# Optimization experiments

Measured on AMD Instinct MI355X. Metric: run time of the kernel, lower is better.

The kernel has to match this reference:

```python
import jax, jax.numpy as jnp
import numpy as np

D_MODEL = 1024
NUM_HEADS = 16
D_K = D_MODEL // NUM_HEADS


def setup_inputs() -> dict:
    key = jax.random.key(0)
    ks = jax.random.split(key, 11)
    s = 1.0 / np.sqrt(D_MODEL)
    inp = {
        "Q": jax.random.normal(ks[0], (2, 2048, D_MODEL), jnp.float32),
        "K": jax.random.normal(ks[1], (2, 2048, D_MODEL), jnp.float32),
        "V": jax.random.normal(ks[2], (2, 2048, D_MODEL), jnp.float32),
        "W_q": jax.random.uniform(ks[3], (D_MODEL, D_MODEL), jnp.float32, -s, s),
        "b_q": jax.random.uniform(ks[4], (D_MODEL,), jnp.float32, -s, s),
        "W_k": jax.random.uniform(ks[5], (D_MODEL, D_MODEL), jnp.float32, -s, s),
        "b_k": jax.random.uniform(ks[6], (D_MODEL,), jnp.float32, -s, s),
        "W_v": jax.random.uniform(ks[7], (D_MODEL, D_MODEL), jnp.float32, -s, s),
        "b_v": jax.random.uniform(ks[8], (D_MODEL,), jnp.float32, -s, s),
        "W_o": jax.random.uniform(ks[9], (D_MODEL, D_MODEL), jnp.float32, -s, s),
        "b_o": jax.random.uniform(ks[10], (D_MODEL,), jnp.float32, -s, s),
    }
    return inp


def reference(Q, K, V, W_q, b_q, W_k, b_k, W_v, b_v, W_o, b_o):
    B, S, _ = Q.shape
    # Linear projections (torch Linear: x @ W.T + b; W here stored as [in, out])
    q = Q @ W_q + b_q
    k = K @ W_k + b_k
    v = V @ W_v + b_v
    # split heads -> [B, H, S, d_k]
    q = q.reshape(B, S, NUM_HEADS, D_K).transpose(0, 2, 1, 3)
    k = k.reshape(B, S, NUM_HEADS, D_K).transpose(0, 2, 1, 3)
    v = v.reshape(B, S, NUM_HEADS, D_K).transpose(0, 2, 1, 3)
    scale = 1.0 / np.sqrt(D_K).astype(np.float32)
    scores = jnp.einsum('bhqd,bhkd->bhqk', q, k) * scale  # [B,H,S,S]
    probs = jax.nn.softmax(scores, axis=-1)
    attn = jnp.einsum('bhqk,bhkd->bhqd', probs, v)  # [B,H,S,d_k]
    attn = attn.transpose(0, 2, 1, 3).reshape(B, S, D_MODEL)
    return attn @ W_o + b_o
```

## Files before the change

kernel.cpp:

```cpp
#include <hip/hip_runtime.h>
#include <math.h>

#define SEQ   2048
#define DM    1024
#define NH    16
#define DK    64
#define MTOT  4096
#define QSCALE 0.18033688011112043f

typedef __bf16 bf16x8 __attribute__((ext_vector_type(8)));
typedef float  f32x4  __attribute__((ext_vector_type(4)));
typedef unsigned short u16;

__device__ __forceinline__ u16 f2bf(float f) {
    unsigned int u = __float_as_uint(f);
    u += 0x7fff + ((u >> 16) & 1);
    return (u16)(u >> 16);
}

__device__ __forceinline__ void async16(const void* g, void* l) {
    __builtin_amdgcn_global_load_lds(
        (const __attribute__((address_space(1))) unsigned int*)(unsigned long long)g,
        (__attribute__((address_space(3))) unsigned int*)(unsigned int)(unsigned long long)l,
        16, 0, 0);
}

__device__ __forceinline__ bf16x8 ld16(const u16* p) {
    bf16x8 v;
    __builtin_memcpy(&v, p, 16);
    return v;
}
__device__ __forceinline__ bf16x8 ld8x2(const u16* p) {
    union { unsigned long long q[2]; bf16x8 v; } u;
    __builtin_memcpy(&u.q[0], p, 8);
    __builtin_memcpy(&u.q[1], p + 4, 8);
    return u.v;
}
__device__ __forceinline__ void st8(u16* p, unsigned int lo, unsigned int hi) {
    unsigned long long q = ((unsigned long long)hi << 32) | lo;
    __builtin_memcpy(p, &q, 8);
}

__global__ __launch_bounds__(256)
void cvt_in(const float* __restrict__ Q, const float* __restrict__ K,
            const float* __restrict__ V, u16* __restrict__ Qb,
            u16* __restrict__ Kb, u16* __restrict__ Vb)
{
    const float* src; u16* dst;
    if (blockIdx.z == 0)      { src = Q; dst = Qb; }
    else if (blockIdx.z == 1) { src = K; dst = Kb; }
    else                      { src = V; dst = Vb; }
    const size_t i = ((size_t)blockIdx.x * 256 + threadIdx.x) * 8;
    float4 a = *(const float4*)&src[i];
    float4 b = *(const float4*)&src[i + 4];
    uint4 o;
    o.x = (unsigned)f2bf(a.x) | ((unsigned)f2bf(a.y) << 16);
    o.y = (unsigned)f2bf(a.z) | ((unsigned)f2bf(a.w) << 16);
    o.z = (unsigned)f2bf(b.x) | ((unsigned)f2bf(b.y) << 16);
    o.w = (unsigned)f2bf(b.z) | ((unsigned)f2bf(b.w) << 16);
    *(uint4*)&dst[i] = o;
}

__global__ __launch_bounds__(256)
void cvt_wt(const float* __restrict__ Wq, const float* __restrict__ Wk,
            const float* __restrict__ Wv, const float* __restrict__ Wo,
            u16* __restrict__ Tq, u16* __restrict__ Tk,
            u16* __restrict__ Tv, u16* __restrict__ To)
{
    const float* W; u16* Wt;
    if (blockIdx.z == 0)      { W = Wq; Wt = Tq; }
    else if (blockIdx.z == 1) { W = Wk; Wt = Tk; }
    else if (blockIdx.z == 2) { W = Wv; Wt = Tv; }
    else                      { W = Wo; Wt = To; }
    __shared__ float Ts[64][65];
    const int t = threadIdx.x;
    const int k0 = blockIdx.x * 64, n0 = blockIdx.y * 64;
#pragma unroll
    for (int p = 0; p < 4; ++p) {
        const int flat = t + p * 256;
        const int r = flat >> 4, c4 = (flat & 15) * 4;
        float4 v = *(const float4*)&W[(size_t)(k0 + r) * DM + n0 + c4];
        Ts[r][c4 + 0] = v.x; Ts[r][c4 + 1] = v.y;
        Ts[r][c4 + 2] = v.z; Ts[r][c4 + 3] = v.w;
    }
    __syncthreads();
#pragma unroll
    for (int p = 0; p < 2; ++p) {
        const int flat = t + p * 256;
        const int n = flat >> 3, kc = (flat & 7) * 8;
        uint4 o;
        o.x = (unsigned)f2bf(Ts[kc + 0][n]) | ((unsigned)f2bf(Ts[kc + 1][n]) << 16);
        o.y = (unsigned)f2bf(Ts[kc + 2][n]) | ((unsigned)f2bf(Ts[kc + 3][n]) << 16);
        o.z = (unsigned)f2bf(Ts[kc + 4][n]) | ((unsigned)f2bf(Ts[kc + 5][n]) << 16);
        o.w = (unsigned)f2bf(Ts[kc + 6][n]) | ((unsigned)f2bf(Ts[kc + 7][n]) << 16);
        *(uint4*)&Wt[(size_t)(n0 + n) * DM + k0 + kc] = o;
    }
}

__global__ __launch_bounds__(256)
void v_transpose(const u16* __restrict__ vn, u16* __restrict__ vt)
{
    __shared__ u16 Ts[64][65];
    const int t = threadIdx.x;
    const int s0 = blockIdx.x * 64, bh = blockIdx.y;
    const size_t nb = (size_t)bh * SEQ * DK;
#pragma unroll
    for (int p = 0; p < 2; ++p) {
        const int flat = t + p * 256;
        const int r = flat >> 3, c = (flat & 7) * 8;
        union { uint4 u; u16 s[8]; } v;
        v.u = *(const uint4*)&vn[nb + (size_t)(s0 + r) * DK + c];
#pragma unroll
        for (int j = 0; j < 8; ++j) Ts[r][c + j] = v.s[j];
    }
    __syncthreads();
#pragma unroll
    for (int p = 0; p < 2; ++p) {
        const int flat = t + p * 256;
        const int d = flat >> 3, sc = (flat & 7) * 8;
        union { uint4 u; u16 s[8]; } v;
#pragma unroll
        for (int j = 0; j < 8; ++j) v.s[j] = Ts[sc + j][d];
        *(uint4*)&vt[nb + (size_t)d * SEQ + s0 + sc] = v.u;
    }
}

template <int SCATTER>
__device__ __forceinline__ void gemm_core(const u16* __restrict__ A,
                                          const u16* __restrict__ Wt,
                                          const float* __restrict__ bias,
                                          void* __restrict__ Out, float scale)
{
    __shared__ u16 As[128 * 32];
    __shared__ u16 Bs[128 * 32];

    const int tid = threadIdx.x;
    const int lane = tid & 63;
    const int wv = __builtin_amdgcn_readfirstlane(tid >> 6);
    const int wm = wv >> 1, wn = wv & 1;
    const int lane15 = lane & 15, quad = lane >> 4;
    const int row0 = blockIdx.x * 128, col0 = blockIdx.y * 128;

    const int arow = lane >> 2;
    const int acol = (lane & 3) * 8;

    f32x4 acc[4][4];
#pragma unroll
    for (int i = 0; i < 4; ++i)
#pragma unroll
        for (int j = 0; j < 4; ++j) acc[i][j] = (f32x4)0.f;

    for (int k0 = 0; k0 < DM; k0 += 32) {
#pragma unroll
        for (int cc = 0; cc < 2; ++cc) {
            const int c = 2 * wv + cc;
            async16(&A[(size_t)(row0 + c * 16 + arow) * DM + k0 + acol],
                    &As[c * 512]);
            async16(&Wt[(size_t)(col0 + c * 16 + arow) * DM + k0 + acol],
                    &Bs[c * 512]);
        }
        __syncthreads();

        bf16x8 af[4];
#pragma unroll
        for (int mi = 0; mi < 4; ++mi)
            af[mi] = ld16(&As[(wm * 64 + mi * 16 + lane15) * 32 + quad * 8]);
#pragma unroll
        for (int ni = 0; ni < 4; ++ni) {
            bf16x8 bfrag = ld16(&Bs[(wn * 64 + ni * 16 + lane15) * 32 + quad * 8]);
#pragma unroll
            for (int mi = 0; mi < 4; ++mi)
                acc[mi][ni] = __builtin_amdgcn_mfma_f32_16x16x32_bf16(
                    af[mi], bfrag, acc[mi][ni], 0, 0, 0);
        }
        __syncthreads();
    }

#pragma unroll
    for (int mi = 0; mi < 4; ++mi) {
        const int mbase = row0 + wm * 64 + mi * 16 + quad * 4;
#pragma unroll
        for (int ni = 0; ni < 4; ++ni) {
            const int n = col0 + wn * 64 + ni * 16 + lane15;
            const float bz = bias[n];
            if (SCATTER) {
                const int h = n >> 6, dk = n & 63;
#pragma unroll
                for (int r = 0; r < 4; ++r) {
                    const int mm = mbase + r;
                    const int b_ = mm >> 11, s = mm & 2047;
                    ((u16*)Out)[(((size_t)(b_ * NH + h)) * SEQ + s) * DK + dk] =
                        f2bf((acc[mi][ni][r] + bz) * scale);
                }
            } else {
#pragma unroll
                for (int r = 0; r < 4; ++r) {
                    const int mm = mbase + r;
                    ((float*)Out)[(size_t)mm * DM + n] = acc[mi][ni][r] + bz;
                }
            }
        }
    }
}

__global__ __launch_bounds__(256)
void qkv_gemm(const u16* __restrict__ Qb, const u16* __restrict__ Kb,
              const u16* __restrict__ Vb,
              const u16* __restrict__ Tq, const u16* __restrict__ Tk,
              const u16* __restrict__ Tv,
              const float* __restrict__ bq, const float* __restrict__ bk,
              const float* __restrict__ bv,
              u16* __restrict__ qw, u16* __restrict__ kw, u16* __restrict__ vw)
{
    if (blockIdx.z == 0)      gemm_core<1>(Qb, Tq, bq, qw, QSCALE);
    else if (blockIdx.z == 1) gemm_core<1>(Kb, Tk, bk, kw, 1.0f);
    else                      gemm_core<1>(Vb, Tv, bv, vw, 1.0f);
}

__global__ __launch_bounds__(256)
void out_gemm(const u16* __restrict__ A, const u16* __restrict__ To,
              const float* __restrict__ bo, float* __restrict__ Out)
{
    gemm_core<0>(A, To, bo, Out, 1.0f);
}

__global__ __launch_bounds__(256, 4)
void attn_mfma(const u16* __restrict__ qw, const u16* __restrict__ kw,
               const u16* __restrict__ vt, u16* __restrict__ attnb)
{
    __shared__ u16 Qs[64 * 68];
    __shared__ u16 Ks[64 * 68];
    __shared__ u16 Vts[64 * 68];
    __shared__ u16 Ps[4][16 * 68];

    const int tid = threadIdx.x;
    const int lane = tid & 63;
    const int wv = tid >> 6;
    const int lane15 = lane & 15, quad = lane >> 4;
    const int bh = blockIdx.x;
    const int q0 = blockIdx.y * 64;
    const size_t base = (size_t)bh * SEQ * DK;

#pragma unroll
    for (int i = 0; i < 2; ++i) {
        const int flat = tid + i * 256;
        const int r = flat >> 3, c = (flat & 7) * 8;
        uint4 v = *(const uint4*)&qw[base + (size_t)(q0 + r) * DK + c];
        st8(&Qs[r * 68 + c], v.x, v.y);
        st8(&Qs[r * 68 + c + 4], v.z, v.w);
    }
    __syncthreads();

    bf16x8 qa[2];
#pragma unroll
    for (int kk = 0; kk < 2; ++kk)
        qa[kk] = ld8x2(&Qs[(wv * 16 + lane15) * 68 + kk * 32 + quad * 8]);

    u16* Pw = &Ps[wv][0];

    f32x4 o_acc[4];
    float lpart[4];
#pragma unroll
    for (int nd = 0; nd < 4; ++nd) o_acc[nd] = (f32x4)0.f;
#pragma unroll
    for (int r = 0; r < 4; ++r) lpart[r] = 0.f;

    for (int c0 = 0; c0 < SEQ; c0 += 64) {
#pragma unroll
        for (int i = 0; i < 2; ++i) {
            const int flat = tid + i * 256;
            const int r = flat >> 3, c = (flat & 7) * 8;
            uint4 kv = *(const uint4*)&kw[base + (size_t)(c0 + r) * DK + c];
            st8(&Ks[r * 68 + c], kv.x, kv.y);
            st8(&Ks[r * 68 + c + 4], kv.z, kv.w);
            uint4 vv = *(const uint4*)&vt[base + (size_t)r * SEQ + c0 + c];
            st8(&Vts[r * 68 + c], vv.x, vv.y);
            st8(&Vts[r * 68 + c + 4], vv.z, vv.w);
        }
        __syncthreads();

        f32x4 s_acc[4];
#pragma unroll
        for (int ni = 0; ni < 4; ++ni) s_acc[ni] = (f32x4)0.f;
#pragma unroll
        for (int ni = 0; ni < 4; ++ni)
#pragma unroll
            for (int kk = 0; kk < 2; ++kk) {
                bf16x8 kb = ld8x2(&Ks[(ni * 16 + lane15) * 68 + kk * 32 + quad * 8]);
                s_acc[ni] = __builtin_amdgcn_mfma_f32_16x16x32_bf16(
                    qa[kk], kb, s_acc[ni], 0, 0, 0);
            }

#pragma unroll
        for (int ni = 0; ni < 4; ++ni) {
#pragma unroll
            for (int r = 0; r < 4; ++r) {
                const float p = exp2f(s_acc[ni][r]);
                lpart[r] += p;
                Pw[(quad * 4 + r) * 68 + ni * 16 + lane15] = f2bf(p);
            }
        }

        bf16x8 pa[2];
#pragma unroll
        for (int kk = 0; kk < 2; ++kk)
            pa[kk] = ld8x2(&Pw[lane15 * 68 + kk * 32 + quad * 8]);
#pragma unroll
        for (int nd = 0; nd < 4; ++nd)
#pragma unroll
            for (int kk = 0; kk < 2; ++kk) {
                bf16x8 vb = ld8x2(&Vts[(nd * 16 + lane15) * 68 + kk * 32 + quad * 8]);
                o_acc[nd] = __builtin_amdgcn_mfma_f32_16x16x32_bf16(
                    pa[kk], vb, o_acc[nd], 0, 0, 0);
            }
        __syncthreads();
    }

#pragma unroll
    for (int r = 0; r < 4; ++r) {
        float l = lpart[r];
        l += __shfl_xor(l, 1);
        l += __shfl_xor(l, 2);
        l += __shfl_xor(l, 4);
        l += __shfl_xor(l, 8);
        lpart[r] = 1.f / l;
    }

    const int b_ = bh >> 4, h = bh & 15;
#pragma unroll
    for (int r = 0; r < 4; ++r) {
        const int srow = q0 + wv * 16 + quad * 4 + r;
#pragma unroll
        for (int nd = 0; nd < 4; ++nd)
            attnb[((size_t)b_ * SEQ + srow) * DM + h * DK + nd * 16 + lane15] =
                f2bf(o_acc[nd][r] * lpart[r]);
    }
}

extern "C" void kernel_launch(void* const* d_in, const int* in_sizes, int n_in,
                              void* d_out, int out_size, void* d_ws, size_t ws_size,
                              hipStream_t stream)
{
    const float* Q  = (const float*)d_in[0];
    const float* K  = (const float*)d_in[1];
    const float* V  = (const float*)d_in[2];
    const float* Wq = (const float*)d_in[3];
    const float* bq = (const float*)d_in[4];
    const float* Wk = (const float*)d_in[5];
    const float* bk = (const float*)d_in[6];
    const float* Wv = (const float*)d_in[7];
    const float* bv = (const float*)d_in[8];
    const float* Wo = (const float*)d_in[9];
    const float* bo = (const float*)d_in[10];
    float* out = (float*)d_out;

    const size_t MB = 1024 * 1024;
    char* w8 = (char*)d_ws;
    u16* Qbf = (u16*)(w8 + 0 * MB);
    u16* Kbf = (u16*)(w8 + 8 * MB);
    u16* Vbf = (u16*)(w8 + 16 * MB);
    u16* Wtq = (u16*)(w8 + 24 * MB);
    u16* Wtk = (u16*)(w8 + 26 * MB);
    u16* Wtv = (u16*)(w8 + 28 * MB);
    u16* Wto = (u16*)(w8 + 30 * MB);
    u16* qw  = (u16*)(w8 + 32 * MB);
    u16* kw  = (u16*)(w8 + 40 * MB);
    u16* vw  = (u16*)(w8 + 48 * MB);
    u16* vtw = (u16*)(w8 + 56 * MB);
    u16* attnb = Qbf;

    cvt_in<<<dim3(2048, 1, 3), 256, 0, stream>>>(Q, K, V, Qbf, Kbf, Vbf);
    cvt_wt<<<dim3(16, 16, 4), 256, 0, stream>>>(Wq, Wk, Wv, Wo,
                                                Wtq, Wtk, Wtv, Wto);
    qkv_gemm<<<dim3(32, 8, 3), 256, 0, stream>>>(Qbf, Kbf, Vbf, Wtq, Wtk, Wtv,
                                                 bq, bk, bv, qw, kw, vw);
    v_transpose<<<dim3(32, 32), 256, 0, stream>>>(vw, vtw);
    attn_mfma<<<dim3(32, 32), 256, 0, stream>>>(qw, kw, vtw, attnb);
    out_gemm<<<dim3(32, 8), 256, 0, stream>>>(attnb, Wto, bo, out);
}
```

Before: 253.0 us.

## Fuse V transpose into QKV epilogue, enlarge attention Q tile, prefetch K/V

The V projection epilogue now writes its output directly in transposed [B,H,dk,S] layout with packed 8-byte stores, which removes the separate v_transpose kernel and its round trip through memory. The attention kernel now handles 128 query rows per block (two 16-row MFMA tiles per wave), so each K/V tile loaded into shared memory is reused twice as much. It also prefetches the next K/V tile into registers while computing on the current one. The output GEMM uses 128x64 tiles to launch twice as many blocks. The trade-off is higher register pressure in attention, since the occupancy hint was dropped, and fewer attention blocks overall.

```diff
diff --git a/kernel.cpp b/kernel.cpp
--- a/kernel.cpp
+++ b/kernel.cpp
@@ -11,6 +11,7 @@
 typedef __bf16 bf16x8 __attribute__((ext_vector_type(8)));
 typedef float  f32x4  __attribute__((ext_vector_type(4)));
 typedef unsigned short u16;
+typedef unsigned long long u64;
 
 __device__ __forceinline__ u16 f2bf(float f) {
     unsigned int u = __float_as_uint(f);
@@ -31,13 +32,13 @@
     return v;
 }
 __device__ __forceinline__ bf16x8 ld8x2(const u16* p) {
-    union { unsigned long long q[2]; bf16x8 v; } u;
+    union { u64 q[2]; bf16x8 v; } u;
     __builtin_memcpy(&u.q[0], p, 8);
     __builtin_memcpy(&u.q[1], p + 4, 8);
     return u.v;
 }
 __device__ __forceinline__ void st8(u16* p, unsigned int lo, unsigned int hi) {
-    unsigned long long q = ((unsigned long long)hi << 32) | lo;
+    u64 q = ((u64)hi << 32) | lo;
     __builtin_memcpy(p, &q, 8);
 }
 
@@ -97,34 +98,6 @@
     }
 }
 
-__global__ __launch_bounds__(256)
-void v_transpose(const u16* __restrict__ vn, u16* __restrict__ vt)
-{
-    __shared__ u16 Ts[64][65];
-    const int t = threadIdx.x;
-    const int s0 = blockIdx.x * 64, bh = blockIdx.y;
-    const size_t nb = (size_t)bh * SEQ * DK;
-#pragma unroll
-    for (int p = 0; p < 2; ++p) {
-        const int flat = t + p * 256;
-        const int r = flat >> 3, c = (flat & 7) * 8;
-        union { uint4 u; u16 s[8]; } v;
-        v.u = *(const uint4*)&vn[nb + (size_t)(s0 + r) * DK + c];
-#pragma unroll
-        for (int j = 0; j < 8; ++j) Ts[r][c + j] = v.s[j];
-    }
-    __syncthreads();
-#pragma unroll
-    for (int p = 0; p < 2; ++p) {
-        const int flat = t + p * 256;
-        const int d = flat >> 3, sc = (flat & 7) * 8;
-        union { uint4 u; u16 s[8]; } v;
-#pragma unroll
-        for (int j = 0; j < 8; ++j) v.s[j] = Ts[sc + j][d];
-        *(uint4*)&vt[nb + (size_t)d * SEQ + s0 + sc] = v.u;
-    }
-}
-
 template <int SCATTER>
 __device__ __forceinline__ void gemm_core(const u16* __restrict__ A,
                                           const u16* __restrict__ Wt,
@@ -183,7 +156,7 @@
         for (int ni = 0; ni < 4; ++ni) {
             const int n = col0 + wn * 64 + ni * 16 + lane15;
             const float bz = bias[n];
-            if (SCATTER) {
+            if (SCATTER == 1) {
                 const int h = n >> 6, dk = n & 63;
 #pragma unroll
                 for (int r = 0; r < 4; ++r) {
@@ -192,6 +165,16 @@
                     ((u16*)Out)[(((size_t)(b_ * NH + h)) * SEQ + s) * DK + dk] =
                         f2bf((acc[mi][ni][r] + bz) * scale);
                 }
+            } else if (SCATTER == 2) {
+                const int h = n >> 6, dk = n & 63;
+                const int b_ = mbase >> 11, s0 = mbase & 2047;
+                u64 q = (u64)f2bf((acc[mi][ni][0] + bz) * scale)
+                      | ((u64)f2bf((acc[mi][ni][1] + bz) * scale) << 16)
+                      | ((u64)f2bf((acc[mi][ni][2] + bz) * scale) << 32)
+                      | ((u64)f2bf((acc[mi][ni][3] + bz) * scale) << 48);
+                u16* dst = (u16*)Out +
+                    (((size_t)(b_ * NH + h)) * DK + dk) * SEQ + s0;
+                __builtin_memcpy(dst, &q, 8);
             } else {
 #pragma unroll
                 for (int r = 0; r < 4; ++r) {
@@ -210,39 +193,98 @@
               const u16* __restrict__ Tv,
               const float* __restrict__ bq, const float* __restrict__ bk,
               const float* __restrict__ bv,
-              u16* __restrict__ qw, u16* __restrict__ kw, u16* __restrict__ vw)
+              u16* __restrict__ qw, u16* __restrict__ kw, u16* __restrict__ vtw)
 {
     if (blockIdx.z == 0)      gemm_core<1>(Qb, Tq, bq, qw, QSCALE);
     else if (blockIdx.z == 1) gemm_core<1>(Kb, Tk, bk, kw, 1.0f);
-    else                      gemm_core<1>(Vb, Tv, bv, vw, 1.0f);
+    else                      gemm_core<2>(Vb, Tv, bv, vtw, 1.0f);
 }
 
 __global__ __launch_bounds__(256)
-void out_gemm(const u16* __restrict__ A, const u16* __restrict__ To,
-              const float* __restrict__ bo, float* __restrict__ Out)
-{
-    gemm_core<0>(A, To, bo, Out, 1.0f);
-}
-
-__global__ __launch_bounds__(256, 4)
+void out_gemm(const u16* __restrict__ A, const u16* __restrict__ Wt,
+              const float* __restrict__ bias, float* __restrict__ Out)
+{
+    __shared__ u16 As[128 * 32];
+    __shared__ u16 Bs[64 * 32];
+
+    const int tid = threadIdx.x;
+    const int lane = tid & 63;
+    const int wv = __builtin_amdgcn_readfirstlane(tid >> 6);
+    const int wm = wv >> 1, wn = wv & 1;
+    const int lane15 = lane & 15, quad = lane >> 4;
+    const int row0 = blockIdx.x * 128, col0 = blockIdx.y * 64;
+
+    const int arow = lane >> 2;
+    const int acol = (lane & 3) * 8;
+
+    f32x4 acc[4][2];
+#pragma unroll
+    for (int i = 0; i < 4; ++i)
+#pragma unroll
+        for (int j = 0; j < 2; ++j) acc[i][j] = (f32x4)0.f;
+
+    for (int k0 = 0; k0 < DM; k0 += 32) {
+#pragma unroll
+        for (int cc = 0; cc < 2; ++cc) {
+            const int c = 2 * wv + cc;
+            async16(&A[(size_t)(row0 + c * 16 + arow) * DM + k0 + acol],
+                    &As[c * 512]);
+        }
+        async16(&Wt[(size_t)(col0 + wv * 16 + arow) * DM + k0 + acol],
+                &Bs[wv * 512]);
+        __syncthreads();
+
+        bf16x8 af[4];
+#pragma unroll
+        for (int mi = 0; mi < 4; ++mi)
+            af[mi] = ld16(&As[(wm * 64 + mi * 16 + lane15) * 32 + quad * 8]);
+#pragma unroll
+        for (int ni = 0; ni < 2; ++ni) {
+            bf16x8 bfrag = ld16(&Bs[(wn * 32 + ni * 16 + lane15) * 32 + quad * 8]);
+#pragma unroll
+            for (int mi = 0; mi < 4; ++mi)
+                acc[mi][ni] = __builtin_amdgcn_mfma_f32_16x16x32_bf16(
+                    af[mi], bfrag, acc[mi][ni], 0, 0, 0);
+        }
+        __syncthreads();
+    }
+
+#pragma unroll
+    for (int mi = 0; mi < 4; ++mi) {
+        const int mbase = row0 + wm * 64 + mi * 16 + quad * 4;
+#pragma unroll
+        for (int ni = 0; ni < 2; ++ni) {
+            const int n = col0 + wn * 32 + ni * 16 + lane15;
+            const float bz = bias[n];
+#pragma unroll
+            for (int r = 0; r < 4; ++r)
+                Out[(size_t)(mbase + r) * DM + n] = acc[mi][ni][r] + bz;
+        }
+    }
+}
+
+__global__ __launch_bounds__(256)
 void attn_mfma(const u16* __restrict__ qw, const u16* __restrict__ kw,
                const u16* __restrict__ vt, u16* __restrict__ attnb)
 {
-    __shared__ u16 Qs[64 * 68];
+    __shared__ u16 Qs[128 * 68];
     __shared__ u16 Ks[64 * 68];
     __shared__ u16 Vts[64 * 68];
-    __shared__ u16 Ps[4][16 * 68];
+    __shared__ u16 Ps[4][32 * 68];
 
     const int tid = threadIdx.x;
     const int lane = tid & 63;
     const int wv = tid >> 6;
     const int lane15 = lane & 15, quad = lane >> 4;
     const int bh = blockIdx.x;
-    const int q0 = blockIdx.y * 64;
+    const int q0 = blockIdx.y * 128;
     const size_t base = (size_t)bh * SEQ * DK;
 
-#pragma unroll
-    for (int i = 0; i < 2; ++i) {
+    const int lr = tid >> 3;
+    const int lc = (tid & 7) * 8;
+
+#pragma unroll
+    for (int i = 0; i < 4; ++i) {
         const int flat = tid + i * 256;
         const int r = flat >> 3, c = (flat & 7) * 8;
         uint4 v = *(const uint4*)&qw[base + (size_t)(q0 + r) * DK + c];
@@ -251,90 +293,129 @@
     }
     __syncthreads();
 
-    bf16x8 qa[2];
-#pragma unroll
-    for (int kk = 0; kk < 2; ++kk)
-        qa[kk] = ld8x2(&Qs[(wv * 16 + lane15) * 68 + kk * 32 + quad * 8]);
+    bf16x8 qa[2][2];
+#pragma unroll
+    for (int mi = 0; mi < 2; ++mi)
+#pragma unroll
+        for (int kk = 0; kk < 2; ++kk)
+            qa[mi][kk] = ld8x2(&Qs[(wv * 32 + mi * 16 + lane15) * 68 +
+                                   kk * 32 + quad * 8]);
 
     u16* Pw = &Ps[wv][0];
 
-    f32x4 o_acc[4];
-    float lpart[4];
-#pragma unroll
-    for (int nd = 0; nd < 4; ++nd) o_acc[nd] = (f32x4)0.f;
-#pragma unroll
-    for (int r = 0; r < 4; ++r) lpart[r] = 0.f;
+    f32x4 o_acc[2][4];
+    float lpart[8];
+#pragma unroll
+    for (int mi = 0; mi < 2; ++mi)
+#pragma unroll
+        for (int nd = 0; nd < 4; ++nd) o_acc[mi][nd] = (f32x4)0.f;
+#pragma unroll
+    for (int r = 0; r < 8; ++r) lpart[r] = 0.f;
+
+#pragma unroll
+    for (int i = 0; i < 2; ++i) {
+        const int r = lr + i * 32, c = lc;
+        uint4 kv = *(const uint4*)&kw[base + (size_t)r * DK + c];
+        st8(&Ks[r * 68 + c], kv.x, kv.y);
+        st8(&Ks[r * 68 + c + 4], kv.z, kv.w);
+        uint4 vv = *(const uint4*)&vt[base + (size_t)r * SEQ + c];
+        st8(&Vts[r * 68 + c], vv.x, vv.y);
+        st8(&Vts[r * 68 + c + 4], vv.z, vv.w);
+    }
+    __syncthreads();
 
     for (int c0 = 0; c0 < SEQ; c0 += 64) {
-#pragma unroll
-        for (int i = 0; i < 2; ++i) {
-            const int flat = tid + i * 256;
-            const int r = flat >> 3, c = (flat & 7) * 8;
-            uint4 kv = *(const uint4*)&kw[base + (size_t)(c0 + r) * DK + c];
-            st8(&Ks[r * 68 + c], kv.x, kv.y);
-            st8(&Ks[r * 68 + c + 4], kv.z, kv.w);
-            uint4 vv = *(const uint4*)&vt[base + (size_t)r * SEQ + c0 + c];
-            st8(&Vts[r * 68 + c], vv.x, vv.y);
-            st8(&Vts[r * 68 + c + 4], vv.z, vv.w);
-        }
-        __syncthreads();
-
-        f32x4 s_acc[4];
-#pragma unroll
-        for (int ni = 0; ni < 4; ++ni) s_acc[ni] = (f32x4)0.f;
+        uint4 kpre[2], vpre[2];
+        const bool more = (c0 + 64 < SEQ);
+        if (more) {
+#pragma unroll
+            for (int i = 0; i < 2; ++i) {
+                const int r = lr + i * 32;
+                kpre[i] = *(const uint4*)&kw[base + (size_t)(c0 + 64 + r) * DK + lc];
+                vpre[i] = *(const uint4*)&vt[base + (size_t)r * SEQ + c0 + 64 + lc];
+            }
+        }
+
+        f32x4 s_acc[2][4];
+#pragma unroll
+        for (int mi = 0; mi < 2; ++mi)
+#pragma unroll
+            for (int ni = 0; ni < 4; ++ni) s_acc[mi][ni] = (f32x4)0.f;
 #pragma unroll
         for (int ni = 0; ni < 4; ++ni)
 #pragma unroll
             for (int kk = 0; kk < 2; ++kk) {
                 bf16x8 kb = ld8x2(&Ks[(ni * 16 + lane15) * 68 + kk * 32 + quad * 8]);
-                s_acc[ni] = __builtin_amdgcn_mfma_f32_16x16x32_bf16(
-                    qa[kk], kb, s_acc[ni], 0, 0, 0);
+#pragma unroll
+                for (int mi = 0; mi < 2; ++mi)
+                    s_acc[mi][ni] = __builtin_amdgcn_mfma_f32_16x16x32_bf16(
+                        qa[mi][kk], kb, s_acc[mi][ni], 0, 0, 0);
             }
 
 #pragma unroll
-        for (int ni = 0; ni < 4; ++ni) {
-#pragma unroll
-            for (int r = 0; r < 4; ++r) {
-                const float p = exp2f(s_acc[ni][r]);
-                lpart[r] += p;
-                Pw[(quad * 4 + r) * 68 + ni * 16 + lane15] = f2bf(p);
-            }
-        }
-
-        bf16x8 pa[2];
-#pragma unroll
-        for (int kk = 0; kk < 2; ++kk)
-            pa[kk] = ld8x2(&Pw[lane15 * 68 + kk * 32 + quad * 8]);
+        for (int mi = 0; mi < 2; ++mi)
+#pragma unroll
+            for (int ni = 0; ni < 4; ++ni)
+#pragma unroll
+                for (int r = 0; r < 4; ++r) {
+                    const float p = exp2f(s_acc[mi][ni][r]);
+                    lpart[mi * 4 + r] += p;
+                    Pw[(mi * 16 + quad * 4 + r) * 68 + ni * 16 + lane15] = f2bf(p);
+                }
+
+        bf16x8 pa[2][2];
+#pragma unroll
+        for (int mi = 0; mi < 2; ++mi)
+#pragma unroll
+            for (int kk = 0; kk < 2; ++kk)
+                pa[mi][kk] = ld8x2(&Pw[(mi * 16 + lane15) * 68 + kk * 32 + quad * 8]);
 #pragma unroll
         for (int nd = 0; nd < 4; ++nd)
 #pragma unroll
             for (int kk = 0; kk < 2; ++kk) {
                 bf16x8 vb = ld8x2(&Vts[(nd * 16 + lane15) * 68 + kk * 32 + quad * 8]);
-                o_acc[nd] = __builtin_amdgcn_mfma_f32_16x16x32_bf16(
-                    pa[kk], vb, o_acc[nd], 0, 0, 0);
+#pragma unroll
+                for (int mi = 0; mi < 2; ++mi)
+                    o_acc[mi][nd] = __builtin_amdgcn_mfma_f32_16x16x32_bf16(
+                        pa[mi][kk], vb, o_acc[mi][nd], 0, 0, 0);
             }
         __syncthreads();
-    }
-
-#pragma unroll
-    for (int r = 0; r < 4; ++r) {
-        float l = lpart[r];
+
+        if (more) {
+#pragma unroll
+            for (int i = 0; i < 2; ++i) {
+                const int r = lr + i * 32, c = lc;
+                st8(&Ks[r * 68 + c], kpre[i].x, kpre[i].y);
+                st8(&Ks[r * 68 + c + 4], kpre[i].z, kpre[i].w);
+                st8(&Vts[r * 68 + c], vpre[i].x, vpre[i].y);
+                st8(&Vts[r * 68 + c + 4], vpre[i].z, vpre[i].w);
+            }
+        }
+        __syncthreads();
+    }
+
+#pragma unroll
+    for (int idx = 0; idx < 8; ++idx) {
+        float l = lpart[idx];
         l += __shfl_xor(l, 1);
         l += __shfl_xor(l, 2);
         l += __shfl_xor(l, 4);
         l += __shfl_xor(l, 8);
-        lpart[r] = 1.f / l;
+        lpart[idx] = 1.f / l;
     }
 
     const int b_ = bh >> 4, h = bh & 15;
 #pragma unroll
-    for (int r = 0; r < 4; ++r) {
-        const int srow = q0 + wv * 16 + quad * 4 + r;
-#pragma unroll
-        for (int nd = 0; nd < 4; ++nd)
-            attnb[((size_t)b_ * SEQ + srow) * DM + h * DK + nd * 16 + lane15] =
-                f2bf(o_acc[nd][r] * lpart[r]);
-    }
+    for (int mi = 0; mi < 2; ++mi)
+#pragma unroll
+        for (int r = 0; r < 4; ++r) {
+            const int srow = q0 + wv * 32 + mi * 16 + quad * 4 + r;
+            const float inv = lpart[mi * 4 + r];
+#pragma unroll
+            for (int nd = 0; nd < 4; ++nd)
+                attnb[((size_t)b_ * SEQ + srow) * DM + h * DK + nd * 16 + lane15] =
+                    f2bf(o_acc[mi][nd][r] * inv);
+        }
 }
 
 extern "C" void kernel_launch(void* const* d_in, const int* in_sizes, int n_in,
@@ -365,16 +446,14 @@
     u16* Wto = (u16*)(w8 + 30 * MB);
     u16* qw  = (u16*)(w8 + 32 * MB);
     u16* kw  = (u16*)(w8 + 40 * MB);
-    u16* vw  = (u16*)(w8 + 48 * MB);
-    u16* vtw = (u16*)(w8 + 56 * MB);
+    u16* vtw = (u16*)(w8 + 48 * MB);
     u16* attnb = Qbf;
 
     cvt_in<<<dim3(2048, 1, 3), 256, 0, stream>>>(Q, K, V, Qbf, Kbf, Vbf);
     cvt_wt<<<dim3(16, 16, 4), 256, 0, stream>>>(Wq, Wk, Wv, Wo,
                                                 Wtq, Wtk, Wtv, Wto);
     qkv_gemm<<<dim3(32, 8, 3), 256, 0, stream>>>(Qbf, Kbf, Vbf, Wtq, Wtk, Wtv,
-                                                 bq, bk, bv, qw, kw, vw);
-    v_transpose<<<dim3(32, 32), 256, 0, stream>>>(vw, vtw);
-    attn_mfma<<<dim3(32, 32), 256, 0, stream>>>(qw, kw, vtw, attnb);
-    out_gemm<<<dim3(32, 8), 256, 0, stream>>>(attnb, Wto, bo, out);
-}
+                                                 bq, bk, bv, qw, kw, vtw);
+    attn_mfma<<<dim3(32, 16), 256, 0, stream>>>(qw, kw, vtw, attnb);
+    out_gemm<<<dim3(32, 16), 256, 0, stream>>>(attnb, Wto, bo, out);
+}
```

New measurement: 244.2 us. 1.04x faster.
